# Kernel tuning notes

Measured on AMD Instinct MI355X. Metric: run time of the kernel, lower is better.

Reference implementation:

```python
import jax, jax.numpy as jnp
import numpy as np

EPS = 1e-6


def setup_inputs() -> dict:
    key = jax.random.key(0)
    ks = jax.random.split(key, 6)
    B, T, C, H, D, M = 1, 2048, 1024, 16, 64, 64
    return {
        "x": jax.random.normal(ks[0], (B, T, C), dtype=jnp.float32),
        "w_qkv": jax.random.normal(ks[1], (C, 3 * C), dtype=jnp.float32) * (1.0 / np.sqrt(C)),
        "b_qkv": jax.random.normal(ks[2], (3 * C,), dtype=jnp.float32) * 0.02,
        "w_out": jax.random.normal(ks[3], (C, C), dtype=jnp.float32) * (1.0 / np.sqrt(C)),
        "b_out": jax.random.normal(ks[4], (C,), dtype=jnp.float32) * 0.02,
        "proj": jax.random.normal(ks[5], (H, D, M), dtype=jnp.float32),
    }


def _feature_map(x, proj):
    # x: [B,H,T,D], proj: [H,D,M] -> [B,H,T,M]
    M = proj.shape[-1]
    p = jnp.einsum("bhtd,hdm->bhtm", x, proj)
    return jax.nn.relu(p) / jnp.sqrt(jnp.float32(M))


def reference(x, w_qkv, b_qkv, w_out, b_out, proj):
    B, T, C = x.shape
    H, D, M = proj.shape
    qkv = x @ w_qkv + b_qkv                        # [B,T,3C]
    q, k, v = jnp.split(qkv, 3, axis=-1)
    # [B,T,C] -> [B,H,T,D]
    to_heads = lambda t: t.reshape(B, T, H, D).transpose(0, 2, 1, 3)
    q, k, v = to_heads(q), to_heads(k), to_heads(v)

    q_prime = _feature_map(q, proj)                # [B,H,T,M]
    k_prime = _feature_map(k, proj)                # [B,H,T,M]

    # causal linear attention: cumulative sum of outer products k' v^T
    kv_prod = jnp.einsum("bhtm,bhtd->bhtmd", k_prime, v)   # [B,H,T,M,D]
    kv_cumsum = jnp.cumsum(kv_prod, axis=2)
    context = jnp.einsum("bhtm,bhtmd->bhtd", q_prime, kv_cumsum)

    k_cumsum = jnp.cumsum(k_prime, axis=2)                   # [B,H,T,M]
    norm = jnp.einsum("bhtm,bhtm->bht", q_prime, k_cumsum)
    out = context / (norm[..., None] + EPS)                  # [B,H,T,D]

    out = out.transpose(0, 2, 1, 3).reshape(B, T, C)
    return out @ w_out + b_out
```

## Files before the change

kernel.cpp:

```cpp
#include <hip/hip_runtime.h>
#include <hip/hip_bf16.h>

#define TT 2048
#define CC 1024
#define HH 16
#define DD 64
#define FM 64
#define NCH 32
#define CL 64
#define N_QKV 3072
#define EPSV 1e-6f

#define OFF_KS  0u
#define OFF_Z   32768u
#define OFF_U16 65536u
#define U_KVT 0u
#define U_QBF 2097152u
#define U_KBF 4194304u
#define U_VT  6291456u
#define U_QP  8388608u
#define U_KP  10485760u
#define U_ST  12582912u
#define U_XBF 14680064u
#define U_WQT 16777216u
#define U_WOT 19922944u

typedef __attribute__((ext_vector_type(8))) short bf16x8;
typedef __attribute__((ext_vector_type(4))) float f32x4;
typedef __attribute__((ext_vector_type(4))) unsigned short u16x4;

__device__ __forceinline__ unsigned short f2bf(float f) {
  unsigned int u = __float_as_uint(f);
  u = (u + 0x7fffu + ((u >> 16) & 1u)) >> 16;
  return (unsigned short)u;
}
__device__ __forceinline__ float bf2f(unsigned short b) {
  return __uint_as_float(((unsigned)b) << 16);
}

__device__ __forceinline__ void gload16(const void* g, void* l) {
  __builtin_amdgcn_global_load_lds(
      (const __attribute__((address_space(1))) unsigned int*)g,
      (__attribute__((address_space(3))) unsigned int*)l, 16, 0, 0);
}

__device__ __forceinline__ void stage_tile64(const unsigned short* g, unsigned rowstride,
                                             unsigned short* lds, int w, int lane) {
  const int l8 = lane >> 3, l7 = lane & 7;
  const int kcg = (l7 ^ l8) * 8;
#pragma unroll
  for (int jj = 0; jj < 2; ++jj) {
    const int inst = w * 2 + jj;
    const int row = inst * 8 + l8;
    gload16(&g[(unsigned)row * rowstride + kcg], &lds[inst * 512]);
  }
}

__device__ __forceinline__ bf16x8 frag64(const unsigned short* lds, int r, int kchunk) {
  const int slot = kchunk ^ (r & 7);
  return *reinterpret_cast<const bf16x8*>(&lds[r * 64 + slot * 8]);
}

__device__ __forceinline__ void transpose64_dev(const float* __restrict__ src,
                                                unsigned short* __restrict__ dst,
                                                int K, int N, int k0, int n0,
                                                float (*T)[68], int tid) {
#pragma unroll
  for (int it = 0; it < 4; ++it) {
    int f = tid + it * 256;
    int r = f >> 4, c4 = (f & 15) * 4;
    float4 v = *reinterpret_cast<const float4*>(&src[(unsigned)(k0 + r) * N + n0 + c4]);
    T[r][c4 + 0] = v.x; T[r][c4 + 1] = v.y;
    T[r][c4 + 2] = v.z; T[r][c4 + 3] = v.w;
  }
  __syncthreads();
#pragma unroll
  for (int it = 0; it < 4; ++it) {
    int f = tid + it * 256;
    int nl = f >> 4, kq = (f & 15) * 4;
    u16x4 o;
#pragma unroll
    for (int j = 0; j < 4; ++j) o[j] = f2bf(T[kq + j][nl]);
    *reinterpret_cast<u16x4*>(&dst[(unsigned)(n0 + nl) * K + k0 + kq]) = o;
  }
}

__global__ __launch_bounds__(256) void k_prep(const float* __restrict__ x,
                                              const float* __restrict__ wq,
                                              const float* __restrict__ wo,
                                              unsigned short* __restrict__ xbf,
                                              unsigned short* __restrict__ wqT,
                                              unsigned short* __restrict__ woT) {
  __shared__ float T[64][68];
  const int tid = threadIdx.x;
  int b = blockIdx.x;
  if (b < 2048) {
    unsigned i = (unsigned)b * 1024u + (unsigned)tid * 4u;
    float4 v = *reinterpret_cast<const float4*>(&x[i]);
    u16x4 o;
    o[0] = f2bf(v.x); o[1] = f2bf(v.y); o[2] = f2bf(v.z); o[3] = f2bf(v.w);
    *reinterpret_cast<u16x4*>(&xbf[i]) = o;
    return;
  }
  b -= 2048;
  if (b < 768) {
    transpose64_dev(wq, wqT, CC, N_QKV, (b / 48) * 64, (b % 48) * 64, T, tid);
    return;
  }
  b -= 768;
  transpose64_dev(wo, woT, CC, CC, (b / 16) * 64, (b % 16) * 64, T, tid);
}

__global__ __launch_bounds__(256) void k_qkv_mfma(const unsigned short* __restrict__ Xbf,
                                                  const unsigned short* __restrict__ WqT,
                                                  const float* __restrict__ bias,
                                                  unsigned short* __restrict__ qbf,
                                                  unsigned short* __restrict__ kbf,
                                                  unsigned short* __restrict__ vt) {
  __shared__ unsigned short LDSU[12288];
  unsigned short* As = LDSU;
  unsigned short* Bs = LDSU + 4096;
  const int tid = threadIdx.x, lane = tid & 63, w = tid >> 6;
  const int wm = w >> 1, wn = w & 1;
  int lin = blockIdx.y * 24 + blockIdx.x;
  int swz = (lin & 7) * 96 + (lin >> 3);
  const int bx = swz % 24, by = swz / 24;
  const int m0b = by * 64, n0b = bx * 128;
  const int l8 = lane >> 3, l7 = lane & 7;
  const int kcg = (l7 ^ l8) * 8;
  f32x4 acc[2][4] = {};
  for (int k0 = 0; k0 < CC; k0 += 64) {
    if (k0) __syncthreads();
#pragma unroll
    for (int jj = 0; jj < 2; ++jj) {
      const int inst = w * 2 + jj;
      const int row = inst * 8 + l8;
      gload16(&Xbf[(unsigned)(m0b + row) * CC + k0 + kcg], &As[inst * 512]);
    }
#pragma unroll
    for (int jj = 0; jj < 4; ++jj) {
      const int inst = w * 4 + jj;
      const int row = inst * 8 + l8;
      gload16(&WqT[(unsigned)(n0b + row) * CC + k0 + kcg], &Bs[inst * 512]);
    }
    __syncthreads();
#pragma unroll
    for (int kk = 0; kk < 2; ++kk) {
      bf16x8 af[2], bg[4];
#pragma unroll
      for (int i = 0; i < 2; ++i) {
        const int r = wm * 32 + i * 16 + (lane & 15);
        const int slot = (kk * 4 + (lane >> 4)) ^ (r & 7);
        af[i] = *reinterpret_cast<const bf16x8*>(&As[r * 64 + slot * 8]);
      }
#pragma unroll
      for (int j = 0; j < 4; ++j) {
        const int r = wn * 64 + j * 16 + (lane & 15);
        const int slot = (kk * 4 + (lane >> 4)) ^ (r & 7);
        bg[j] = *reinterpret_cast<const bf16x8*>(&Bs[r * 64 + slot * 8]);
      }
#pragma unroll
      for (int i = 0; i < 2; ++i)
#pragma unroll
        for (int j = 0; j < 4; ++j)
          acc[i][j] = __builtin_amdgcn_mfma_f32_16x16x32_bf16(af[i], bg[j],
                                                              acc[i][j], 0, 0, 0);
    }
  }
  const int n0w = n0b + wn * 64;
  const int sel = n0w >> 10;
  const int h = (n0w & 1023) >> 6;
  const int t0w = m0b + wm * 32;
  float bvj[4];
#pragma unroll
  for (int j = 0; j < 4; ++j) bvj[j] = bias[n0w + j * 16 + (lane & 15)];
  __syncthreads();
  unsigned short* myT = LDSU + w * 2048;
#pragma unroll
  for (int i = 0; i < 2; ++i)
#pragma unroll
    for (int j = 0; j < 4; ++j) {
      const int d = j * 16 + (lane & 15);
#pragma unroll
      for (int r = 0; r < 4; ++r) {
        const int t = i * 16 + (lane >> 4) * 4 + r;
        myT[t * 64 + (((d >> 3) ^ (t & 7)) << 3) + (d & 7)] = f2bf(acc[i][j][r] + bvj[j]);
      }
    }
  if (sel == 2) {
#pragma unroll
    for (int q = 0; q < 4; ++q) {
      const int cid = q * 64 + lane;
      const int d = cid >> 2, tc = cid & 3;
      bf16x8 o;
#pragma unroll
      for (int e = 0; e < 8; ++e) {
        const int t = tc * 8 + e;
        o[e] = (short)myT[t * 64 + (((d >> 3) ^ (t & 7)) << 3) + (d & 7)];
      }
      *reinterpret_cast<bf16x8*>(&vt[((unsigned)h * 64 + d) * TT + t0w + tc * 8]) = o;
    }
  } else {
    unsigned short* dst0 = (sel ? kbf : qbf) + ((unsigned)h * TT + (unsigned)t0w) * 64u;
#pragma unroll
    for (int q = 0; q < 4; ++q) {
      const int cid = q * 64 + lane;
      const int t = cid >> 3, dc = cid & 7;
      bf16x8 o = *reinterpret_cast<const bf16x8*>(&myT[t * 64 + ((dc ^ (t & 7)) << 3)]);
      *reinterpret_cast<bf16x8*>(&dst0[(unsigned)cid * 8]) = o;
    }
  }
}

__global__ __launch_bounds__(256) void k_feat(const float* __restrict__ proj,
                                              const unsigned short* __restrict__ qbf,
                                              const unsigned short* __restrict__ kbf,
                                              const unsigned short* __restrict__ vt,
                                              unsigned short* __restrict__ qp,
                                              unsigned short* __restrict__ kp,
                                              unsigned short* __restrict__ kvt,
                                              float* __restrict__ ksum) {
  __shared__ unsigned short Xs[4096];
  __shared__ float Pj[4096];
  __shared__ unsigned short Os[4096];
  __shared__ unsigned short VTs[4096];
  const int tid = threadIdx.x, lane = tid & 63, w = tid >> 6;
  const int c = blockIdx.x, h = blockIdx.y, which = blockIdx.z;
  const unsigned short* src = (which ? kbf : qbf) + ((unsigned)h * TT + c * 64) * 64;
  stage_tile64(src, 64, Xs, w, lane);
  if (which) stage_tile64(vt + (unsigned)h * 64 * TT + (unsigned)c * 64, TT, VTs, w, lane);
#pragma unroll
  for (int it = 0; it < 4; ++it) {
    const unsigned idx = (unsigned)(tid + it * 256) * 4u;
    *reinterpret_cast<f32x4*>(&Pj[idx]) =
        *reinterpret_cast<const f32x4*>(&proj[(unsigned)h * 4096 + idx]);
  }
  __syncthreads();
  const int mrow = w * 16 + (lane & 15);
  bf16x8 af[2];
#pragma unroll
  for (int kk = 0; kk < 2; ++kk)
#pragma unroll
    for (int e = 0; e < 8; ++e) {
      const int d = (lane >> 4) * 8 + kk * 32 + e;
      af[kk][e] = (short)f2bf(Pj[d * 64 + mrow]);
    }
  f32x4 accf[4] = {};
#pragma unroll
  for (int j = 0; j < 4; ++j)
#pragma unroll
    for (int kk = 0; kk < 2; ++kk)
      accf[j] = __builtin_amdgcn_mfma_f32_16x16x32_bf16(
          af[kk], frag64(Xs, j * 16 + (lane & 15), kk * 4 + (lane >> 4)), accf[j], 0, 0, 0);
#pragma unroll
  for (int j = 0; j < 4; ++j)
#pragma unroll
    for (int r = 0; r < 4; ++r) {
      float v = accf[j][r];
      accf[j][r] = (v > 0.f ? v : 0.f) * 0.125f;
    }
#pragma unroll
  for (int j = 0; j < 4; ++j) {
    const int t = j * 16 + (lane & 15);
#pragma unroll
    for (int r = 0; r < 4; ++r) {
      const int m = w * 16 + (lane >> 4) * 4 + r;
      Os[t * 64 + (((m >> 3) ^ (t & 7)) * 8) + (m & 7)] = f2bf(accf[j][r]);
    }
  }
  if (which) {
    float rs[4];
#pragma unroll
    for (int r = 0; r < 4; ++r) {
      float s = accf[0][r] + accf[1][r] + accf[2][r] + accf[3][r];
#pragma unroll
      for (int off = 1; off < 16; off <<= 1) s += __shfl_xor(s, off, 64);
      rs[r] = s;
    }
    if ((lane & 15) == 0) {
#pragma unroll
      for (int r = 0; r < 4; ++r) {
        const int m = w * 16 + (lane >> 4) * 4 + r;
        ksum[((unsigned)h * NCH + c) * 64u + m] = rs[r];
      }
    }
  }
  __syncthreads();
  unsigned short* dst = (which ? kp : qp) + ((unsigned)h * TT + c * 64) * 64;
  {
    const int t = tid >> 2;
#pragma unroll
    for (int q = 0; q < 2; ++q) {
      const int chunk = (tid & 3) * 2 + q;
      bf16x8 vle = *reinterpret_cast<const bf16x8*>(&Os[t * 64 + ((chunk ^ (t & 7)) * 8)]);
      *reinterpret_cast<bf16x8*>(&dst[t * 64 + chunk * 8]) = vle;
    }
  }
  if (which) {
    const int m = w * 16 + (lane & 15);
    bf16x8 afm[2];
#pragma unroll
    for (int kk = 0; kk < 2; ++kk)
#pragma unroll
      for (int e = 0; e < 8; ++e) {
        const int t = kk * 32 + (lane >> 4) * 8 + e;
        afm[kk][e] = (short)Os[t * 64 + (((m >> 3) ^ (t & 7)) << 3) + (m & 7)];
      }
    f32x4 acckv[4] = {};
#pragma unroll
    for (int j = 0; j < 4; ++j)
#pragma unroll
      for (int kk = 0; kk < 2; ++kk)
        acckv[j] = __builtin_amdgcn_mfma_f32_16x16x32_bf16(
            afm[kk], frag64(VTs, j * 16 + (lane & 15), kk * 4 + (lane >> 4)), acckv[j], 0, 0, 0);
    unsigned short* dkv = kvt + ((unsigned)h * NCH + c) * 4096u;
#pragma unroll
    for (int j = 0; j < 4; ++j) {
      const int d = j * 16 + (lane & 15);
      const int mq = w * 16 + (lane >> 4) * 4;
      u16x4 o;
#pragma unroll
      for (int r = 0; r < 4; ++r) o[r] = f2bf(acckv[j][r]);
      *reinterpret_cast<u16x4*>(&dkv[(unsigned)d * 64 + mq]) = o;
    }
  }
}

__global__ __launch_bounds__(256) void k_prefix(const unsigned short* __restrict__ kvt,
                                                const float* __restrict__ ksum,
                                                unsigned short* __restrict__ st,
                                                float* __restrict__ z) {
  const int h = blockIdx.y;
  const unsigned e = blockIdx.x * 256u + threadIdx.x;
  float run = 0.f;
#pragma unroll
  for (int c = 0; c < NCH; ++c) {
    const unsigned idx = ((unsigned)h * NCH + c) * 4096u + e;
    st[idx] = f2bf(run);
    run += bf2f(kvt[idx]);
  }
  if (blockIdx.x == 0 && threadIdx.x < 64) {
    float zr = 0.f;
#pragma unroll
    for (int c = 0; c < NCH; ++c) {
      const unsigned idx = ((unsigned)h * NCH + c) * 64u + threadIdx.x;
      z[idx] = zr;
      zr += ksum[idx];
    }
  }
}

__global__ __launch_bounds__(256) void k_attn(const unsigned short* __restrict__ qp,
                                              const unsigned short* __restrict__ kp,
                                              const unsigned short* __restrict__ vt,
                                              const unsigned short* __restrict__ st,
                                              const float* __restrict__ z,
                                              unsigned short* __restrict__ attnb) {
  __shared__ unsigned short QPs[4096];
  __shared__ unsigned short KPs[4096];
  __shared__ unsigned short VTs[4096];
  __shared__ unsigned short STs[4096];
  __shared__ float zsm[64];
  __shared__ float nsm[64];
  const int tid = threadIdx.x, lane = tid & 63, w = tid >> 6;
  const int c = blockIdx.x, h = blockIdx.y;
  stage_tile64(qp + ((unsigned)h * TT + c * 64) * 64, 64, QPs, w, lane);
  stage_tile64(kp + ((unsigned)h * TT + c * 64) * 64, 64, KPs, w, lane);
  stage_tile64(vt + (unsigned)h * 64 * TT + (unsigned)c * 64, TT, VTs, w, lane);
  stage_tile64(st + ((unsigned)h * NCH + c) * 4096u, 64, STs, w, lane);
  if (tid < 64) zsm[tid] = z[((unsigned)h * NCH + c) * 64u + tid];
  __syncthreads();
  const int tr = w * 16 + (lane & 15);
  bf16x8 afq[2];
#pragma unroll
  for (int kk = 0; kk < 2; ++kk) afq[kk] = frag64(QPs, tr, kk * 4 + (lane >> 4));
  f32x4 accA[4] = {};
#pragma unroll
  for (int j = 0; j < 4; ++j)
#pragma unroll
    for (int kk = 0; kk < 2; ++kk)
      accA[j] = __builtin_amdgcn_mfma_f32_16x16x32_bf16(
          afq[kk], frag64(KPs, j * 16 + (lane & 15), kk * 4 + (lane >> 4)), accA[j], 0, 0, 0);
  float rs[4] = {0.f, 0.f, 0.f, 0.f};
#pragma unroll
  for (int j = 0; j < 4; ++j) {
    const int s = j * 16 + (lane & 15);
#pragma unroll
    for (int r = 0; r < 4; ++r) {
      const int t = w * 16 + (lane >> 4) * 4 + r;
      float v = (s <= t) ? accA[j][r] : 0.f;
      accA[j][r] = v;
      rs[r] += v;
    }
  }
#pragma unroll
  for (int r = 0; r < 4; ++r)
#pragma unroll
    for (int off = 1; off < 16; off <<= 1) rs[r] += __shfl_xor(rs[r], off, 64);
  __syncthreads();
  if ((lane & 15) == 0) {
#pragma unroll
    for (int r = 0; r < 4; ++r) nsm[w * 16 + (lane >> 4) * 4 + r] = rs[r];
  }
#pragma unroll
  for (int j = 0; j < 4; ++j) {
    const int s = j * 16 + (lane & 15);
#pragma unroll
    for (int r = 0; r < 4; ++r) {
      const int t = w * 16 + (lane >> 4) * 4 + r;
      KPs[t * 64 + (((s >> 3) ^ (t & 7)) * 8) + (s & 7)] = f2bf(accA[j][r]);
    }
  }
  __syncthreads();
  {
    const int t = tid >> 2, part = tid & 3;
    float qz = 0.f;
#pragma unroll
    for (int mm = 0; mm < 16; ++mm) {
      const int m = part * 16 + mm;
      qz += bf2f(QPs[t * 64 + (((m >> 3) ^ (t & 7)) * 8) + (m & 7)]) * zsm[m];
    }
    qz += __shfl_xor(qz, 1, 64);
    qz += __shfl_xor(qz, 2, 64);
    if (part == 0) nsm[t] += qz + EPSV;
  }
  bf16x8 afa[2];
#pragma unroll
  for (int kk = 0; kk < 2; ++kk) afa[kk] = frag64(KPs, tr, kk * 4 + (lane >> 4));
  f32x4 acc[4] = {};
#pragma unroll
  for (int j = 0; j < 4; ++j) {
    const int br = j * 16 + (lane & 15);
#pragma unroll
    for (int kk = 0; kk < 2; ++kk) {
      acc[j] = __builtin_amdgcn_mfma_f32_16x16x32_bf16(
          afa[kk], frag64(VTs, br, kk * 4 + (lane >> 4)), acc[j], 0, 0, 0);
      acc[j] = __builtin_amdgcn_mfma_f32_16x16x32_bf16(
          afq[kk], frag64(STs, br, kk * 4 + (lane >> 4)), acc[j], 0, 0, 0);
    }
  }
  __syncthreads();
#pragma unroll
  for (int j = 0; j < 4; ++j) {
    const int d = j * 16 + (lane & 15);
#pragma unroll
    for (int r = 0; r < 4; ++r) {
      const int t = w * 16 + (lane >> 4) * 4 + r;
      attnb[(unsigned)(c * 64 + t) * CC + h * 64 + d] = f2bf(acc[j][r] / nsm[t]);
    }
  }
}

__global__ __launch_bounds__(256) void k_out_mfma(const unsigned short* __restrict__ Abf,
                                                  const unsigned short* __restrict__ WoT,
                                                  const float* __restrict__ bias,
                                                  float* __restrict__ out) {
  __shared__ unsigned short As[4096];
  __shared__ unsigned short Bs[4096];
  const int tid = threadIdx.x, lane = tid & 63, w = tid >> 6;
  const int wm = w >> 1, wn = w & 1;
  int lin = blockIdx.y * 16 + blockIdx.x;
  int swz = (lin & 7) * 64 + (lin >> 3);
  const int bx = swz & 15, by = swz >> 4;
  const int m0 = by * 64, n0 = bx * 64;
  const int l8 = lane >> 3, l7 = lane & 7;
  const int kcg = (l7 ^ l8) * 8;
  f32x4 acc[2][2] = {};
  for (int k0 = 0; k0 < CC; k0 += 64) {
    if (k0) __syncthreads();
#pragma unroll
    for (int jj = 0; jj < 2; ++jj) {
      const int inst = w * 2 + jj;
      const int row = inst * 8 + l8;
      gload16(&Abf[(unsigned)(m0 + row) * CC + k0 + kcg], &As[inst * 512]);
      gload16(&WoT[(unsigned)(n0 + row) * CC + k0 + kcg], &Bs[inst * 512]);
    }
    __syncthreads();
#pragma unroll
    for (int kk = 0; kk < 2; ++kk) {
      bf16x8 af[2], bg[2];
#pragma unroll
      for (int i = 0; i < 2; ++i) {
        const int r = wm * 32 + i * 16 + (lane & 15);
        const int slot = (kk * 4 + (lane >> 4)) ^ (r & 7);
        af[i] = *reinterpret_cast<const bf16x8*>(&As[r * 64 + slot * 8]);
      }
#pragma unroll
      for (int j = 0; j < 2; ++j) {
        const int r = wn * 32 + j * 16 + (lane & 15);
        const int slot = (kk * 4 + (lane >> 4)) ^ (r & 7);
        bg[j] = *reinterpret_cast<const bf16x8*>(&Bs[r * 64 + slot * 8]);
      }
#pragma unroll
      for (int i = 0; i < 2; ++i)
#pragma unroll
        for (int j = 0; j < 2; ++j)
          acc[i][j] = __builtin_amdgcn_mfma_f32_16x16x32_bf16(af[i], bg[j],
                                                              acc[i][j], 0, 0, 0);
    }
  }
#pragma unroll
  for (int i = 0; i < 2; ++i) {
#pragma unroll
    for (int j = 0; j < 2; ++j) {
      const int n = n0 + wn * 32 + j * 16 + (lane & 15);
      const float bv = bias[n];
#pragma unroll
      for (int r = 0; r < 4; ++r) {
        const int m = m0 + wm * 32 + i * 16 + (lane >> 4) * 4 + r;
        out[(unsigned)m * CC + n] = acc[i][j][r] + bv;
      }
    }
  }
}

extern "C" void kernel_launch(void* const* d_in, const int* in_sizes, int n_in,
                              void* d_out, int out_size, void* d_ws, size_t ws_size,
                              hipStream_t stream) {
  const float* x = (const float*)d_in[0];
  const float* w_qkv = (const float*)d_in[1];
  const float* b_qkv = (const float*)d_in[2];
  const float* w_out = (const float*)d_in[3];
  const float* b_out = (const float*)d_in[4];
  const float* proj = (const float*)d_in[5];
  float* ws = (float*)d_ws;
  float* out = (float*)d_out;
  float* ksum = ws + OFF_KS;
  float* zf = ws + OFF_Z;
  unsigned short* ub = (unsigned short*)(ws + OFF_U16);
  unsigned short* kvt = ub + U_KVT;
  unsigned short* qbf = ub + U_QBF;
  unsigned short* kbf = ub + U_KBF;
  unsigned short* vt = ub + U_VT;
  unsigned short* qp = ub + U_QP;
  unsigned short* kp = ub + U_KP;
  unsigned short* st = ub + U_ST;
  unsigned short* xbf = ub + U_XBF;
  unsigned short* wqT = ub + U_WQT;
  unsigned short* woT = ub + U_WOT;
  unsigned short* attnb = xbf;
  dim3 blk(256, 1, 1);
  k_prep<<<dim3(3072), blk, 0, stream>>>(x, w_qkv, w_out, xbf, wqT, woT);
  k_qkv_mfma<<<dim3(N_QKV / 128, TT / 64), blk, 0, stream>>>(xbf, wqT, b_qkv, qbf, kbf, vt);
  k_feat<<<dim3(NCH, HH, 2), blk, 0, stream>>>(proj, qbf, kbf, vt, qp, kp, kvt, ksum);
  k_prefix<<<dim3(16, HH), blk, 0, stream>>>(kvt, ksum, st, zf);
  k_attn<<<dim3(NCH, HH), blk, 0, stream>>>(qp, kp, vt, st, zf, attnb);
  k_out_mfma<<<dim3(CC / 64, TT / 64), blk, 0, stream>>>(attnb, woT, b_out, out);
}
```

Measured before the change: 70.53 us.

## Fuse random-feature projection and ReLU into QKV GEMM epilogue

The QKV GEMM epilogue now applies the per-head feature projection (an MFMA against a pre-transposed bf16 proj) and the ReLU scaling directly, so it writes q' and k' instead of raw q and k. The old feature kernel is replaced by a smaller chunk-KV kernel that only reads k' and v to form per-chunk K'V products and k sums. This removes a round trip of q/k through global memory and a launch over twice as many blocks. The cost is extra MFMA work and registers in the GEMM epilogue, plus a small transpose of proj in the prep kernel.

```diff
diff --git a/kernel.cpp b/kernel.cpp
--- a/kernel.cpp
+++ b/kernel.cpp
@@ -15,8 +15,7 @@
 #define OFF_Z   32768u
 #define OFF_U16 65536u
 #define U_KVT 0u
-#define U_QBF 2097152u
-#define U_KBF 4194304u
+#define U_PROJT 2097152u
 #define U_VT  6291456u
 #define U_QP  8388608u
 #define U_KP  10485760u
@@ -88,9 +87,11 @@
 __global__ __launch_bounds__(256) void k_prep(const float* __restrict__ x,
                                               const float* __restrict__ wq,
                                               const float* __restrict__ wo,
+                                              const float* __restrict__ proj,
                                               unsigned short* __restrict__ xbf,
                                               unsigned short* __restrict__ wqT,
-                                              unsigned short* __restrict__ woT) {
+                                              unsigned short* __restrict__ woT,
+                                              unsigned short* __restrict__ projT) {
   __shared__ float T[64][68];
   const int tid = threadIdx.x;
   int b = blockIdx.x;
@@ -108,14 +109,20 @@
     return;
   }
   b -= 768;
-  transpose64_dev(wo, woT, CC, CC, (b / 16) * 64, (b % 16) * 64, T, tid);
+  if (b < 256) {
+    transpose64_dev(wo, woT, CC, CC, (b / 16) * 64, (b % 16) * 64, T, tid);
+    return;
+  }
+  b -= 256;
+  transpose64_dev(proj + (unsigned)b * 4096u, projT + (unsigned)b * 4096u, 64, 64, 0, 0, T, tid);
 }
 
 __global__ __launch_bounds__(256) void k_qkv_mfma(const unsigned short* __restrict__ Xbf,
                                                   const unsigned short* __restrict__ WqT,
                                                   const float* __restrict__ bias,
-                                                  unsigned short* __restrict__ qbf,
-                                                  unsigned short* __restrict__ kbf,
+                                                  const unsigned short* __restrict__ projT,
+                                                  unsigned short* __restrict__ qp,
+                                                  unsigned short* __restrict__ kp,
                                                   unsigned short* __restrict__ vt) {
   __shared__ unsigned short LDSU[12288];
   unsigned short* As = LDSU;
@@ -200,129 +207,95 @@
       }
       *reinterpret_cast<bf16x8*>(&vt[((unsigned)h * 64 + d) * TT + t0w + tc * 8]) = o;
     }
-  } else {
-    unsigned short* dst0 = (sel ? kbf : qbf) + ((unsigned)h * TT + (unsigned)t0w) * 64u;
-#pragma unroll
-    for (int q = 0; q < 4; ++q) {
-      const int cid = q * 64 + lane;
-      const int t = cid >> 3, dc = cid & 7;
-      bf16x8 o = *reinterpret_cast<const bf16x8*>(&myT[t * 64 + ((dc ^ (t & 7)) << 3)]);
-      *reinterpret_cast<bf16x8*>(&dst0[(unsigned)cid * 8]) = o;
-    }
-  }
-}
-
-__global__ __launch_bounds__(256) void k_feat(const float* __restrict__ proj,
-                                              const unsigned short* __restrict__ qbf,
-                                              const unsigned short* __restrict__ kbf,
-                                              const unsigned short* __restrict__ vt,
-                                              unsigned short* __restrict__ qp,
-                                              unsigned short* __restrict__ kp,
-                                              unsigned short* __restrict__ kvt,
-                                              float* __restrict__ ksum) {
+    return;
+  }
+  const unsigned short* pjt = projT + (unsigned)h * 4096u;
+  bf16x8 aq[2][2], bp[4][2];
+#pragma unroll
+  for (int jm = 0; jm < 4; ++jm)
+#pragma unroll
+    for (int kk = 0; kk < 2; ++kk)
+      bp[jm][kk] = *reinterpret_cast<const bf16x8*>(
+          &pjt[(unsigned)(jm * 16 + (lane & 15)) * 64 + kk * 32 + (lane >> 4) * 8]);
+#pragma unroll
+  for (int i = 0; i < 2; ++i)
+#pragma unroll
+    for (int kk = 0; kk < 2; ++kk)
+      aq[i][kk] = frag64(myT, i * 16 + (lane & 15), kk * 4 + (lane >> 4));
+  f32x4 accp[2][4] = {};
+#pragma unroll
+  for (int i = 0; i < 2; ++i)
+#pragma unroll
+    for (int jm = 0; jm < 4; ++jm)
+#pragma unroll
+      for (int kk = 0; kk < 2; ++kk)
+        accp[i][jm] = __builtin_amdgcn_mfma_f32_16x16x32_bf16(aq[i][kk], bp[jm][kk],
+                                                              accp[i][jm], 0, 0, 0);
+#pragma unroll
+  for (int i = 0; i < 2; ++i)
+#pragma unroll
+    for (int jm = 0; jm < 4; ++jm) {
+      const int m = jm * 16 + (lane & 15);
+#pragma unroll
+      for (int r = 0; r < 4; ++r) {
+        const int t = i * 16 + (lane >> 4) * 4 + r;
+        float v = accp[i][jm][r];
+        v = (v > 0.f ? v : 0.f) * 0.125f;
+        myT[t * 64 + (((m >> 3) ^ (t & 7)) << 3) + (m & 7)] = f2bf(v);
+      }
+    }
+  unsigned short* dst0 = (sel ? kp : qp) + ((unsigned)h * TT + (unsigned)t0w) * 64u;
+#pragma unroll
+  for (int q = 0; q < 4; ++q) {
+    const int cid = q * 64 + lane;
+    const int t = cid >> 3, mc = cid & 7;
+    bf16x8 o = *reinterpret_cast<const bf16x8*>(&myT[t * 64 + ((mc ^ (t & 7)) << 3)]);
+    *reinterpret_cast<bf16x8*>(&dst0[(unsigned)cid * 8]) = o;
+  }
+}
+
+__global__ __launch_bounds__(256) void k_chunkkv(const unsigned short* __restrict__ kp,
+                                                 const unsigned short* __restrict__ vt,
+                                                 unsigned short* __restrict__ kvt,
+                                                 float* __restrict__ ksum) {
   __shared__ unsigned short Xs[4096];
-  __shared__ float Pj[4096];
-  __shared__ unsigned short Os[4096];
   __shared__ unsigned short VTs[4096];
   const int tid = threadIdx.x, lane = tid & 63, w = tid >> 6;
-  const int c = blockIdx.x, h = blockIdx.y, which = blockIdx.z;
-  const unsigned short* src = (which ? kbf : qbf) + ((unsigned)h * TT + c * 64) * 64;
-  stage_tile64(src, 64, Xs, w, lane);
-  if (which) stage_tile64(vt + (unsigned)h * 64 * TT + (unsigned)c * 64, TT, VTs, w, lane);
-#pragma unroll
-  for (int it = 0; it < 4; ++it) {
-    const unsigned idx = (unsigned)(tid + it * 256) * 4u;
-    *reinterpret_cast<f32x4*>(&Pj[idx]) =
-        *reinterpret_cast<const f32x4*>(&proj[(unsigned)h * 4096 + idx]);
-  }
-  __syncthreads();
-  const int mrow = w * 16 + (lane & 15);
-  bf16x8 af[2];
+  const int c = blockIdx.x, h = blockIdx.y;
+  stage_tile64(kp + ((unsigned)h * TT + c * 64) * 64, 64, Xs, w, lane);
+  stage_tile64(vt + (unsigned)h * 64 * TT + (unsigned)c * 64, TT, VTs, w, lane);
+  __syncthreads();
+  const int m = w * 16 + (lane & 15);
+  bf16x8 afm[2];
+  float ks = 0.f;
 #pragma unroll
   for (int kk = 0; kk < 2; ++kk)
 #pragma unroll
     for (int e = 0; e < 8; ++e) {
-      const int d = (lane >> 4) * 8 + kk * 32 + e;
-      af[kk][e] = (short)f2bf(Pj[d * 64 + mrow]);
-    }
-  f32x4 accf[4] = {};
+      const int t = kk * 32 + (lane >> 4) * 8 + e;
+      unsigned short u = Xs[t * 64 + (((m >> 3) ^ (t & 7)) << 3) + (m & 7)];
+      afm[kk][e] = (short)u;
+      ks += bf2f(u);
+    }
+  ks += __shfl_xor(ks, 16, 64);
+  ks += __shfl_xor(ks, 32, 64);
+  if (lane < 16) ksum[((unsigned)h * NCH + c) * 64u + m] = ks;
+  f32x4 acckv[4] = {};
 #pragma unroll
   for (int j = 0; j < 4; ++j)
 #pragma unroll
     for (int kk = 0; kk < 2; ++kk)
-      accf[j] = __builtin_amdgcn_mfma_f32_16x16x32_bf16(
-          af[kk], frag64(Xs, j * 16 + (lane & 15), kk * 4 + (lane >> 4)), accf[j], 0, 0, 0);
-#pragma unroll
-  for (int j = 0; j < 4; ++j)
-#pragma unroll
-    for (int r = 0; r < 4; ++r) {
-      float v = accf[j][r];
-      accf[j][r] = (v > 0.f ? v : 0.f) * 0.125f;
-    }
+      acckv[j] = __builtin_amdgcn_mfma_f32_16x16x32_bf16(
+          afm[kk], frag64(VTs, j * 16 + (lane & 15), kk * 4 + (lane >> 4)), acckv[j], 0, 0, 0);
+  unsigned short* dkv = kvt + ((unsigned)h * NCH + c) * 4096u;
 #pragma unroll
   for (int j = 0; j < 4; ++j) {
-    const int t = j * 16 + (lane & 15);
-#pragma unroll
-    for (int r = 0; r < 4; ++r) {
-      const int m = w * 16 + (lane >> 4) * 4 + r;
-      Os[t * 64 + (((m >> 3) ^ (t & 7)) * 8) + (m & 7)] = f2bf(accf[j][r]);
-    }
-  }
-  if (which) {
-    float rs[4];
-#pragma unroll
-    for (int r = 0; r < 4; ++r) {
-      float s = accf[0][r] + accf[1][r] + accf[2][r] + accf[3][r];
-#pragma unroll
-      for (int off = 1; off < 16; off <<= 1) s += __shfl_xor(s, off, 64);
-      rs[r] = s;
-    }
-    if ((lane & 15) == 0) {
-#pragma unroll
-      for (int r = 0; r < 4; ++r) {
-        const int m = w * 16 + (lane >> 4) * 4 + r;
-        ksum[((unsigned)h * NCH + c) * 64u + m] = rs[r];
-      }
-    }
-  }
-  __syncthreads();
-  unsigned short* dst = (which ? kp : qp) + ((unsigned)h * TT + c * 64) * 64;
-  {
-    const int t = tid >> 2;
-#pragma unroll
-    for (int q = 0; q < 2; ++q) {
-      const int chunk = (tid & 3) * 2 + q;
-      bf16x8 vle = *reinterpret_cast<const bf16x8*>(&Os[t * 64 + ((chunk ^ (t & 7)) * 8)]);
-      *reinterpret_cast<bf16x8*>(&dst[t * 64 + chunk * 8]) = vle;
-    }
-  }
-  if (which) {
-    const int m = w * 16 + (lane & 15);
-    bf16x8 afm[2];
-#pragma unroll
-    for (int kk = 0; kk < 2; ++kk)
-#pragma unroll
-      for (int e = 0; e < 8; ++e) {
-        const int t = kk * 32 + (lane >> 4) * 8 + e;
-        afm[kk][e] = (short)Os[t * 64 + (((m >> 3) ^ (t & 7)) << 3) + (m & 7)];
-      }
-    f32x4 acckv[4] = {};
-#pragma unroll
-    for (int j = 0; j < 4; ++j)
-#pragma unroll
-      for (int kk = 0; kk < 2; ++kk)
-        acckv[j] = __builtin_amdgcn_mfma_f32_16x16x32_bf16(
-            afm[kk], frag64(VTs, j * 16 + (lane & 15), kk * 4 + (lane >> 4)), acckv[j], 0, 0, 0);
-    unsigned short* dkv = kvt + ((unsigned)h * NCH + c) * 4096u;
-#pragma unroll
-    for (int j = 0; j < 4; ++j) {
-      const int d = j * 16 + (lane & 15);
-      const int mq = w * 16 + (lane >> 4) * 4;
-      u16x4 o;
-#pragma unroll
-      for (int r = 0; r < 4; ++r) o[r] = f2bf(acckv[j][r]);
-      *reinterpret_cast<u16x4*>(&dkv[(unsigned)d * 64 + mq]) = o;
-    }
+    const int d = j * 16 + (lane & 15);
+    const int mq = w * 16 + (lane >> 4) * 4;
+    u16x4 o;
+#pragma unroll
+    for (int r = 0; r < 4; ++r) o[r] = f2bf(acckv[j][r]);
+    *reinterpret_cast<u16x4*>(&dkv[(unsigned)d * 64 + mq]) = o;
   }
 }
 
@@ -529,8 +502,7 @@
   float* zf = ws + OFF_Z;
   unsigned short* ub = (unsigned short*)(ws + OFF_U16);
   unsigned short* kvt = ub + U_KVT;
-  unsigned short* qbf = ub + U_QBF;
-  unsigned short* kbf = ub + U_KBF;
+  unsigned short* projT = ub + U_PROJT;
   unsigned short* vt = ub + U_VT;
   unsigned short* qp = ub + U_QP;
   unsigned short* kp = ub + U_KP;
@@ -540,9 +512,10 @@
   unsigned short* woT = ub + U_WOT;
   unsigned short* attnb = xbf;
   dim3 blk(256, 1, 1);
-  k_prep<<<dim3(3072), blk, 0, stream>>>(x, w_qkv, w_out, xbf, wqT, woT);
-  k_qkv_mfma<<<dim3(N_QKV / 128, TT / 64), blk, 0, stream>>>(xbf, wqT, b_qkv, qbf, kbf, vt);
-  k_feat<<<dim3(NCH, HH, 2), blk, 0, stream>>>(proj, qbf, kbf, vt, qp, kp, kvt, ksum);
+  k_prep<<<dim3(3088), blk, 0, stream>>>(x, w_qkv, w_out, proj, xbf, wqT, woT, projT);
+  k_qkv_mfma<<<dim3(N_QKV / 128, TT / 64), blk, 0, stream>>>(xbf, wqT, b_qkv, projT,
+                                                             qp, kp, vt);
+  k_chunkkv<<<dim3(NCH, HH), blk, 0, stream>>>(kp, vt, kvt, ksum);
   k_prefix<<<dim3(16, HH), blk, 0, stream>>>(kvt, ksum, st, zf);
   k_attn<<<dim3(NCH, HH), blk, 0, stream>>>(qp, kp, vt, st, zf, attnb);
   k_out_mfma<<<dim3(CC / 64, TT / 64), blk, 0, stream>>>(attnb, woT, b_out, out);
```

After: 68.92 us. 1.02x faster.
